# Kernel tuning notes

Measured on AMD Instinct MI355X. Metric: run time of the kernel, lower is better.

The kernel has to match this reference:

```python
import jax, jax.numpy as jnp
import numpy as np
import math

D_MODEL = 1024
D_INNER = 2048
D_HALF = D_INNER // 2
D_STATE = 16
D_CONV = 4
DT_RANK = 64
B_SZ = 4
L = 2048


def _dw_conv(x, w, b):
    # x: (b, l, c), w: (k, 1, c) depthwise, SAME padding
    y = jax.lax.conv_general_dilated(
        x, w, window_strides=(1,), padding='SAME',
        feature_group_count=x.shape[-1],
        dimension_numbers=('NWC', 'WIO', 'NWC'))
    return y + b


def _selective_scan(u, delta, A, Bc, Cc, D):
    # u, delta: (b, l, d); Bc, Cc: (b, l, n); A: (d, n); D: (d,)
    b, l, d = u.shape
    n = A.shape[1]

    def step(h, inp):
        d_t, u_t, B_t, C_t = inp  # (b,d), (b,d), (b,n), (b,n)
        dA = jnp.exp(d_t[..., None] * A)                     # (b,d,n)
        h = dA * h + (d_t * u_t)[..., None] * B_t[:, None, :]
        y = jnp.einsum('bdn,bn->bd', h, C_t)
        return h, y

    h0 = jnp.zeros((b, d, n), u.dtype)
    xs = (jnp.moveaxis(delta, 1, 0), jnp.moveaxis(u, 1, 0),
          jnp.moveaxis(Bc, 1, 0), jnp.moveaxis(Cc, 1, 0))
    _, ys = jax.lax.scan(step, h0, xs)                       # (l,b,d)
    return jnp.moveaxis(ys, 0, 1) + u * D


def setup_inputs() -> dict:
    key = jax.random.key(0)
    ks = jax.random.split(key, 12)
    x = jax.random.normal(ks[0], (B_SZ, L, D_MODEL), jnp.float32)
    W_in = jax.random.normal(ks[1], (D_MODEL, D_INNER), jnp.float32) * (D_MODEL ** -0.5)
    conv_x_w = jax.random.normal(ks[2], (D_CONV, 1, D_HALF), jnp.float32) * (D_CONV ** -0.5)
    conv_x_b = jnp.zeros((D_HALF,), jnp.float32)
    conv_z_w = jax.random.normal(ks[3], (D_CONV, 1, D_HALF), jnp.float32) * (D_CONV ** -0.5)
    conv_z_b = jnp.zeros((D_HALF,), jnp.float32)
    W_xdbl = jax.random.normal(ks[4], (D_HALF, DT_RANK + 2 * D_STATE), jnp.float32) * (D_HALF ** -0.5)
    dt_init_std = DT_RANK ** -0.5  # dt_scale = 1.0
    W_dt = jax.random.uniform(ks[5], (DT_RANK, D_HALF), jnp.float32, -dt_init_std, dt_init_std)
    rand_vals = jax.random.uniform(ks[6], (D_HALF,))
    dt_bias = jnp.exp(rand_vals * (math.log(0.1) - math.log(0.001)) + math.log(0.001))
    dt_bias = jnp.clip(dt_bias, 1e-4)
    inv_dt = dt_bias + jnp.log(-jnp.expm1(-dt_bias))
    D = jnp.ones((D_HALF,), jnp.float32)
    W_out = jax.random.normal(ks[7], (D_INNER, D_MODEL), jnp.float32) * (D_INNER ** -0.5)
    b_out = jnp.zeros((D_MODEL,), jnp.float32)
    return dict(x=x, W_in=W_in, conv_x_w=conv_x_w, conv_x_b=conv_x_b,
                conv_z_w=conv_z_w, conv_z_b=conv_z_b, W_xdbl=W_xdbl,
                W_dt=W_dt, inv_dt=inv_dt, D=D, W_out=W_out, b_out=b_out)


def reference(x, W_in, conv_x_w, conv_x_b, conv_z_w, conv_z_b, W_xdbl,
              W_dt, inv_dt, D, W_out, b_out):
    xz = x @ W_in                                            # (b,l,d_inner), no bias
    xs, z = jnp.split(xz, 2, axis=-1)                        # (b,l,d_half) each
    # A = -exp(log(arange(1..N))) tiled over channels
    A = -jnp.tile(jnp.arange(1, D_STATE + 1, dtype=jnp.float32), (D_HALF, 1))  # (d,n)
    xs = jax.nn.silu(_dw_conv(xs, conv_x_w, conv_x_b))
    z = jax.nn.silu(_dw_conv(z, conv_z_w, conv_z_b))
    x_dbl = xs @ W_xdbl                                      # (b,l,dt_rank+2n)
    dt_low, Bc, Cc = jnp.split(x_dbl, [DT_RANK, DT_RANK + D_STATE], axis=-1)
    dt = dt_low @ W_dt + inv_dt                              # Dense with bias_init=inv_dt
    delta = jax.nn.softplus(dt + inv_dt)                     # scan adds delta_bias=inv_dt again (faithful)
    y = _selective_scan(xs, delta, A, Bc, Cc, D)             # (b,l,d_half)
    y = jnp.concatenate([y, z], axis=-1)                     # (b,l,d_inner)
    return y @ W_out + b_out
```

## Files before the change

### kernel.cpp

```cpp
#include <hip/hip_runtime.h>
#include <hip/hip_bf16.h>
#include <math.h>

#define B_SZ 4
#define LSEQ 2048
#define DM 1024
#define DI 2048
#define DH 1024
#define DS 16
#define DTR 64
#define RTOT 96
#define MROWS (B_SZ * LSEQ)

#define NCH 32
#define CHUNK 64

typedef short bf8_t __attribute__((ext_vector_type(8)));
typedef float f4_t __attribute__((ext_vector_type(4)));

__device__ __forceinline__ unsigned short f2bfbits(float v) {
  __hip_bfloat16 h = __float2bfloat16(v);
  return *(unsigned short*)&h;
}
__device__ __forceinline__ float bfu_lo(unsigned int v) {
  unsigned int x = v << 16;
  return *(float*)&x;
}
__device__ __forceinline__ float bfu_hi(unsigned int v) {
  unsigned int x = v & 0xffff0000u;
  return *(float*)&x;
}

__device__ __forceinline__ void gl_lds16(const void* g, void* l) {
  __builtin_amdgcn_global_load_lds(
      (const __attribute__((address_space(1))) unsigned int*)g,
      (__attribute__((address_space(3))) unsigned int*)l,
      16, 0, 0);
}
__device__ __forceinline__ void gl_lds16_nt(const void* g, void* l) {
  __builtin_amdgcn_global_load_lds(
      (const __attribute__((address_space(1))) unsigned int*)g,
      (__attribute__((address_space(3))) unsigned int*)l,
      16, 0, 2);
}

__device__ __forceinline__ void ld8f(const float* p, unsigned short* d) {
  const float4 a = ((const float4*)p)[0];
  const float4 b = ((const float4*)p)[1];
  d[0] = f2bfbits(a.x); d[1] = f2bfbits(a.y); d[2] = f2bfbits(a.z); d[3] = f2bfbits(a.w);
  d[4] = f2bfbits(b.x); d[5] = f2bfbits(b.y); d[6] = f2bfbits(b.z); d[7] = f2bfbits(b.w);
}

#define VMCNT(n) asm volatile("s_waitcnt vmcnt(" #n ")" ::: "memory")
#define LGKM0 asm volatile("s_waitcnt lgkmcnt(0)" ::: "memory")

__global__ void probe_kernel(const unsigned short* __restrict__ p, int* __restrict__ flag) {
  int lane = threadIdx.x;
  int sane = 0;
#pragma unroll
  for (int j = 0; j < 4; j++) {
    unsigned short lo = p[(lane * 4 + j) * 2];
    int e = (lo >> 7) & 0xFF;
    sane += (e <= 130) ? 1 : 0;
  }
  sane += __shfl_xor(sane, 1, 64);
  sane += __shfl_xor(sane, 2, 64);
  sane += __shfl_xor(sane, 4, 64);
  sane += __shfl_xor(sane, 8, 64);
  sane += __shfl_xor(sane, 16, 64);
  sane += __shfl_xor(sane, 32, 64);
  if (lane == 0) *flag = (sane >= 220) ? 1 : 0;
}

__global__ __launch_bounds__(256) void cast_kernel(
    const int* __restrict__ flag, const float* __restrict__ x,
    unsigned short* __restrict__ xbf) {
  if (*flag == 1) return;
  int i = (blockIdx.x * 256 + threadIdx.x) * 8;
  unsigned short d[8];
  ld8f(x + i, d);
  *(uint4*)&xbf[i] = *(uint4*)d;
}

#define PREP_TOT 78848
__global__ __launch_bounds__(256) void prep_kernel(
    const int* __restrict__ flag,
    const void* s0, const void* s1, const void* s2, const void* s3,
    const void* s4, const void* s5, const void* s6, const void* s7,
    float* __restrict__ out) {
  int i = blockIdx.x * 256 + threadIdx.x;
  if (i >= PREP_TOT) return;
  const void* src; int off;
  if      (i < 4096)   { src = s0; off = i; }
  else if (i < 5120)   { src = s1; off = i - 4096; }
  else if (i < 9216)   { src = s2; off = i - 5120; }
  else if (i < 10240)  { src = s3; off = i - 9216; }
  else if (i < 75776)  { src = s4; off = i - 10240; }
  else if (i < 76800)  { src = s5; off = i - 75776; }
  else if (i < 77824)  { src = s6; off = i - 76800; }
  else                 { src = s7; off = i - 77824; }
  float v = (*flag == 1) ? __bfloat162float(((const __hip_bfloat16*)src)[off])
                         : ((const float*)src)[off];
  out[i] = v;
}

__global__ __launch_bounds__(256) void transpose_kernel(
    const int* __restrict__ flag, const void* __restrict__ W,
    unsigned short* __restrict__ Wt, int K, int N) {
  __shared__ unsigned short tile[32][33];
  int n0 = blockIdx.x * 32, k0 = blockIdx.y * 32;
  int c = threadIdx.x & 31, r8 = threadIdx.x >> 5;
  bool isbf = (*flag == 1);
#pragma unroll
  for (int p = 0; p < 4; p++) {
    int r = r8 + p * 8;
    unsigned short v;
    if (isbf) v = ((const unsigned short*)W)[(size_t)(k0 + r) * N + n0 + c];
    else      v = f2bfbits(((const float*)W)[(size_t)(k0 + r) * N + n0 + c]);
    tile[r][c] = v;
  }
  __syncthreads();
#pragma unroll
  for (int p = 0; p < 4; p++) {
    int r = r8 + p * 8;
    Wt[(size_t)(n0 + r) * K + k0 + c] = tile[c][r];
  }
}

__global__ __launch_bounds__(256) void transpose_pad_kernel(
    const int* __restrict__ flag, const void* __restrict__ W,
    unsigned short* __restrict__ Wt) {
  __shared__ unsigned short tile[32][33];
  int n0 = blockIdx.x * 32, k0 = blockIdx.y * 32;
  int c = threadIdx.x & 31, r8 = threadIdx.x >> 5;
  bool isbf = (*flag == 1);
#pragma unroll
  for (int p = 0; p < 4; p++) {
    int r = r8 + p * 8;
    unsigned short v = 0;
    if (n0 + c < RTOT) {
      if (isbf) v = ((const unsigned short*)W)[(size_t)(k0 + r) * RTOT + n0 + c];
      else      v = f2bfbits(((const float*)W)[(size_t)(k0 + r) * RTOT + n0 + c]);
    }
    tile[r][c] = v;
  }
  __syncthreads();
#pragma unroll
  for (int p = 0; p < 4; p++) {
    int r = r8 + p * 8;
    Wt[(size_t)(n0 + r) * DH + k0 + c] = tile[c][r];
  }
}

template <int BN, bool OUT_BY_FLAG>
__global__ __launch_bounds__(512, 2) void gemm_bk32(
    const int* __restrict__ flag,
    const unsigned short* __restrict__ A1, const unsigned short* __restrict__ A0,
    const unsigned short* __restrict__ Bt,
    const float* __restrict__ bias, void* __restrict__ C,
    int N, int K) {
  extern __shared__ __align__(16) unsigned short lds[];
  constexpr int A_BUF = 256 * 32;
  constexpr int B_BUF = BN * 32;
  constexpr int B_OFF = 4 * A_BUF;
  constexpr int NF = BN / 64;
  constexpr int NB_LD = BN / 128;

  const int flagv = *flag;
  const unsigned short* Ap = (flagv == 1) ? A1 : A0;

  const int tid = threadIdx.x;
  const int lane = tid & 63;
  const int wave = tid >> 6;
  const int quad = lane >> 4;
  const int l16 = lane & 15;
  const int wm = wave >> 2;
  const int wn = wave & 3;

  const int NB = gridDim.x, MB = gridDim.y;
  int L = blockIdx.y * NB + blockIdx.x;
  int xcd = L & 7;
  int w = L >> 3;
  int m_band = xcd * (MB >> 3) + (w / NB);
  int n_blk = w % NB;
  const int m0 = m_band * 256;
  const int n0 = n_blk * BN;

  const int NT = K >> 5;

  f4_t acc[8][NF] = {};

  auto stage = [&](int kt) {
    const int buf = kt & 3;
    const int k0 = kt * 32;
    unsigned short* Ad = lds + buf * A_BUF;
#pragma unroll
    for (int j = 0; j < 2; j++) {
      int ch = tid + j * 512;
      int mi = ch >> 2, s = ch & 3;
      int ki = s ^ ((mi >> 1) & 3);
      gl_lds16_nt(Ap + (size_t)(m0 + mi) * K + k0 + ki * 8,
                  Ad + (j * 512 + wave * 64) * 8);
    }
    unsigned short* Bd = lds + B_OFF + buf * B_BUF;
#pragma unroll
    for (int j = 0; j < NB_LD; j++) {
      int ch = tid + j * 512;
      int ni = ch >> 2, s = ch & 3;
      int ki = s ^ ((ni >> 1) & 3);
      gl_lds16(Bt + (size_t)(n0 + ni) * K + k0 + ki * 8,
               Bd + (j * 512 + wave * 64) * 8);
    }
  };

  stage(0); stage(1); stage(2);

  for (int t = 0; t < NT; t++) {
    if (t + 2 < NT) {
      if constexpr (NF == 4) VMCNT(8); else VMCNT(6);
    } else if (t + 1 < NT) {
      if constexpr (NF == 4) VMCNT(4); else VMCNT(3);
    } else {
      VMCNT(0);
    }
    __builtin_amdgcn_s_barrier();

    const unsigned short* Ac = lds + (t & 3) * A_BUF;
    const unsigned short* Bc = lds + B_OFF + (t & 3) * B_BUF;
    bf8_t af[8], bfr[NF];
#pragma unroll
    for (int ti = 0; ti < 8; ti++) {
      int r = wm * 128 + ti * 16 + l16;
      af[ti] = *(const bf8_t*)&Ac[(r * 4 + (quad ^ ((r >> 1) & 3))) * 8];
    }
#pragma unroll
    for (int tj = 0; tj < NF; tj++) {
      int rn = wn * (BN / 4) + tj * 16 + l16;
      bfr[tj] = *(const bf8_t*)&Bc[(rn * 4 + (quad ^ ((rn >> 1) & 3))) * 8];
    }
    if (t + 3 < NT) stage(t + 3);

    LGKM0;
    __builtin_amdgcn_sched_barrier(0);
    __builtin_amdgcn_s_setprio(1);
#pragma unroll
    for (int ti = 0; ti < 8; ti++)
#pragma unroll
      for (int tj = 0; tj < NF; tj++)
        acc[ti][tj] = __builtin_amdgcn_mfma_f32_16x16x32_bf16(
            af[ti], bfr[tj], acc[ti][tj], 0, 0, 0);
    __builtin_amdgcn_s_setprio(0);
    __builtin_amdgcn_s_barrier();
  }

#pragma unroll
  for (int ti = 0; ti < 8; ti++) {
#pragma unroll
    for (int tj = 0; tj < NF; tj++) {
      int col = n0 + wn * (BN / 4) + tj * 16 + l16;
      float bv = bias ? bias[col] : 0.f;
#pragma unroll
      for (int r = 0; r < 4; r++) {
        int row = m0 + wm * 128 + ti * 16 + quad * 4 + r;
        float v = acc[ti][tj][r] + bv;
        if constexpr (!OUT_BY_FLAG) {
          __builtin_nontemporal_store(f2bfbits(v),
              (unsigned short*)C + (size_t)row * N + col);
        } else {
          if (flagv == 1)
            __builtin_nontemporal_store(f2bfbits(v),
                (unsigned short*)C + (size_t)row * N + col);
          else
            __builtin_nontemporal_store(v, (float*)C + (size_t)row * N + col);
        }
      }
    }
  }
}

__global__ __launch_bounds__(256) void xdbl_kernel(
    const unsigned short* __restrict__ A, const unsigned short* __restrict__ Bt,
    float* __restrict__ xdbl) {
  const int tid = threadIdx.x;
  const int wave = tid >> 6;
  const int lane = tid & 63;
  const int quad = lane >> 4;
  const int l16 = lane & 15;
  const int m0 = blockIdx.x * 32 + (wave & 1) * 16;
  const int c0 = (wave >> 1) * 48;

  f4_t acc[3] = {};
  const unsigned short* Ar = A + (size_t)(m0 + l16) * DH + quad * 8;
  const unsigned short* B0 = Bt + (size_t)(c0 + l16) * DH + quad * 8;
  const unsigned short* B1 = Bt + (size_t)(c0 + 16 + l16) * DH + quad * 8;
  const unsigned short* B2 = Bt + (size_t)(c0 + 32 + l16) * DH + quad * 8;

#pragma unroll 4
  for (int k0 = 0; k0 < DH; k0 += 32) {
    bf8_t af = *(const bf8_t*)(Ar + k0);
    bf8_t b0 = *(const bf8_t*)(B0 + k0);
    bf8_t b1 = *(const bf8_t*)(B1 + k0);
    bf8_t b2 = *(const bf8_t*)(B2 + k0);
    acc[0] = __builtin_amdgcn_mfma_f32_16x16x32_bf16(af, b0, acc[0], 0, 0, 0);
    acc[1] = __builtin_amdgcn_mfma_f32_16x16x32_bf16(af, b1, acc[1], 0, 0, 0);
    acc[2] = __builtin_amdgcn_mfma_f32_16x16x32_bf16(af, b2, acc[2], 0, 0, 0);
  }

#pragma unroll
  for (int tj = 0; tj < 3; tj++) {
    int col = c0 + tj * 16 + l16;
#pragma unroll
    for (int r = 0; r < 4; r++) {
      int row = m0 + quad * 4 + r;
      xdbl[(size_t)row * RTOT + col] = acc[tj][r];
    }
  }
}

__global__ __launch_bounds__(256) void conv_silu_kernel(
    const unsigned short* __restrict__ xz,
    const float* __restrict__ wx, const float* __restrict__ bx,
    const float* __restrict__ wz, const float* __restrict__ bz,
    unsigned short* __restrict__ xs_bf, unsigned short* __restrict__ cat) {
  int gid = blockIdx.x * 256 + threadIdx.x;
  int cg = gid & 127;
  int c0 = cg * 8;
  int m = gid >> 7;
  int t = m & (LSEQ - 1);
  float ax[8], az[8];
#pragma unroll
  for (int i = 0; i < 8; i++) { ax[i] = bx[c0 + i]; az[i] = bz[c0 + i]; }
#pragma unroll
  for (int j = 0; j < 4; j++) {
    int tt = t - 1 + j;
    if (tt < 0 || tt >= LSEQ) continue;
    size_t row = (size_t)(m - t + tt);
    uint4 vx = *(const uint4*)&xz[row * DI + c0];
    uint4 vz = *(const uint4*)&xz[row * DI + DH + c0];
    const unsigned int* px = (const unsigned int*)&vx;
    const unsigned int* pz = (const unsigned int*)&vz;
#pragma unroll
    for (int q = 0; q < 4; q++) {
      float x0 = bfu_lo(px[q]), x1 = bfu_hi(px[q]);
      float z0 = bfu_lo(pz[q]), z1 = bfu_hi(pz[q]);
      ax[q * 2]     = fmaf(wx[j * DH + c0 + q * 2], x0, ax[q * 2]);
      ax[q * 2 + 1] = fmaf(wx[j * DH + c0 + q * 2 + 1], x1, ax[q * 2 + 1]);
      az[q * 2]     = fmaf(wz[j * DH + c0 + q * 2], z0, az[q * 2]);
      az[q * 2 + 1] = fmaf(wz[j * DH + c0 + q * 2 + 1], z1, az[q * 2 + 1]);
    }
  }
  unsigned short sx[8], sz[8];
#pragma unroll
  for (int i = 0; i < 8; i++) {
    float vx = ax[i] / (1.f + __expf(-ax[i]));
    float vz = az[i] / (1.f + __expf(-az[i]));
    sx[i] = f2bfbits(vx);
    sz[i] = f2bfbits(vz);
  }
  *(uint4*)&xs_bf[(size_t)m * DH + c0] = *(uint4*)sx;
  *(uint4*)&cat[(size_t)m * DI + DH + c0] = *(uint4*)sz;
}

__global__ __launch_bounds__(256) void delta_kernel(
    const float* __restrict__ xdbl, const float* __restrict__ Wdt,
    const float* __restrict__ inv_dt, const unsigned short* __restrict__ xs,
    unsigned int* __restrict__ du) {
  const int d = blockIdx.x * 256 + threadIdx.x;
  const int m0 = blockIdx.y * 8;
  __shared__ float xr[8][DTR];
#pragma unroll
  for (int i = 0; i < 2; i++) {
    int e = threadIdx.x + i * 256;
    xr[e >> 6][e & 63] = xdbl[(size_t)(m0 + (e >> 6)) * RTOT + (e & 63)];
  }
  __syncthreads();
  float acc[8];
#pragma unroll
  for (int i = 0; i < 8; i++) acc[i] = 0.f;
  for (int rr = 0; rr < DTR; rr++) {
    float w = Wdt[(size_t)rr * DH + d];
#pragma unroll
    for (int i = 0; i < 8; i++) acc[i] = fmaf(xr[i][rr], w, acc[i]);
  }
  const float bias2 = 2.f * inv_dt[d];
#pragma unroll
  for (int i = 0; i < 8; i++) {
    float v = acc[i] + bias2;
    float sp = (v > 0.f) ? (v + log1pf(__expf(-v))) : log1pf(__expf(v));
    unsigned int lo = f2bfbits(sp);
    unsigned int hi = xs[(size_t)(m0 + i) * DH + d];
    du[(size_t)(m0 + i) * DH + d] = lo | (hi << 16);
  }
}

__global__ __launch_bounds__(256) void scan_pass1(
    const unsigned int* __restrict__ du, const float* __restrict__ xdbl,
    float* __restrict__ Echunks, float* __restrict__ hp) {
  const int tid = threadIdx.x;
  const int d = blockIdx.x * 256 + tid;
  const int c = blockIdx.y, b = blockIdx.z;
  const int row0 = b * LSEQ + c * CHUNK;
  __shared__ float sBC[CHUNK][32];
#pragma unroll
  for (int i = 0; i < 2; i++) {
    int task = tid + i * 256;
    int r = task >> 3, seg = task & 7;
    *(float4*)&sBC[r][seg * 4] =
        *(const float4*)&xdbl[(size_t)(row0 + r) * RTOT + DTR + seg * 4];
  }
  __syncthreads();
  float h[16];
#pragma unroll
  for (int n = 0; n < 16; n++) h[n] = 0.f;
  float E = 1.f;
  for (int t = 0; t < CHUNK; t++) {
    unsigned int v = du[(size_t)(row0 + t) * DH + d];
    float dt = bfu_lo(v), ut = bfu_hi(v);
    float e = __expf(-dt);
    E *= e;
    float dv = dt * ut;
    float p = 1.f;
#pragma unroll
    for (int n = 0; n < 16; n++) {
      p *= e;
      h[n] = fmaf(p, h[n], dv * sBC[t][n]);
    }
  }
  Echunks[((size_t)c * B_SZ + b) * DH + d] = E;
#pragma unroll
  for (int n = 0; n < 16; n++)
    hp[(((size_t)c * B_SZ + b) * 16 + n) * DH + d] = h[n];
}

__global__ __launch_bounds__(256) void scan_pass2(
    const float* __restrict__ Echunks, const float* __restrict__ hp,
    float* __restrict__ hs) {
  int t = blockIdx.x * 256 + threadIdx.x;
  int d = t & 1023;
  int n = (t >> 10) & 15;
  int b = t >> 14;
  float h = 0.f;
  const int k0 = n + 1;
  for (int c = 0; c < NCH; c++) {
    float E = Echunks[((size_t)c * B_SZ + b) * DH + d];
    float a = 1.f, base = E;
    int k = k0;
#pragma unroll
    for (int i = 0; i < 5; i++) {
      if (k & 1) a *= base;
      base *= base;
      k >>= 1;
    }
    size_t idx = (((size_t)c * B_SZ + b) * 16 + n) * DH + d;
    hs[idx] = h;
    h = fmaf(a, h, hp[idx]);
  }
}

__global__ __launch_bounds__(256) void scan_pass3(
    const unsigned int* __restrict__ du, const float* __restrict__ xdbl,
    const float* __restrict__ hs, const float* __restrict__ Dvec,
    __hip_bfloat16* __restrict__ cat) {
  const int tid = threadIdx.x;
  const int d = blockIdx.x * 256 + tid;
  const int c = blockIdx.y, b = blockIdx.z;
  const int row0 = b * LSEQ + c * CHUNK;
  __shared__ float sBC[CHUNK][32];
#pragma unroll
  for (int i = 0; i < 2; i++) {
    int task = tid + i * 256;
    int r = task >> 3, seg = task & 7;
    *(float4*)&sBC[r][seg * 4] =
        *(const float4*)&xdbl[(size_t)(row0 + r) * RTOT + DTR + seg * 4];
  }
  __syncthreads();
  float h[16];
#pragma unroll
  for (int n = 0; n < 16; n++)
    h[n] = hs[(((size_t)c * B_SZ + b) * 16 + n) * DH + d];
  const float Dd = Dvec[d];
  for (int t = 0; t < CHUNK; t++) {
    unsigned int v = du[(size_t)(row0 + t) * DH + d];
    float dt = bfu_lo(v), ut = bfu_hi(v);
    float e = __expf(-dt);
    float dv = dt * ut;
    float p = 1.f, y = 0.f;
#pragma unroll
    for (int n = 0; n < 16; n++) {
      p *= e;
      h[n] = fmaf(p, h[n], dv * sBC[t][n]);
      y = fmaf(h[n], sBC[t][16 + n], y);
    }
    y = fmaf(ut, Dd, y);
    cat[(size_t)(row0 + t) * DI + d] = __float2bfloat16(y);
  }
}

extern "C" void kernel_launch(void* const* d_in, const int* in_sizes, int n_in,
                              void* d_out, int out_size, void* d_ws, size_t ws_size,
                              hipStream_t stream) {
  char* ws = (char*)d_ws;
  __hip_bfloat16* xz  = (__hip_bfloat16*)(ws);
  unsigned int* du    = (unsigned int*)(ws);
  __hip_bfloat16* xs  = (__hip_bfloat16*)(ws + ((size_t)32 << 20));
  unsigned short* xbf = (unsigned short*)(ws + ((size_t)48 << 20));
  __hip_bfloat16* cat = (__hip_bfloat16*)(ws + ((size_t)64 << 20));
  float* xdbl         = (float*)(ws + ((size_t)96 << 20));
  float* Echunks      = (float*)(ws + ((size_t)99 << 20));
  float* hp           = (float*)(ws + ((size_t)100 << 20));
  float* hs           = (float*)(ws + ((size_t)108 << 20));
  unsigned short* Wt_in  = (unsigned short*)(ws + ((size_t)116 << 20));
  unsigned short* Wt_out = (unsigned short*)(ws + ((size_t)120 << 20));
  unsigned short* Wxt    = (unsigned short*)(ws + ((size_t)124 << 20));
  float* cw           = (float*)(ws + ((size_t)125 << 20));
  int* flag           = (int*)(ws + ((size_t)126 << 20));

  const float* conv_xwf = cw + 0;
  const float* conv_xbf = cw + 4096;
  const float* conv_zwf = cw + 5120;
  const float* conv_zbf = cw + 9216;
  const float* Wdtf     = cw + 10240;
  const float* inv_dtf  = cw + 75776;
  const float* Df       = cw + 76800;
  const float* b_outf   = cw + 77824;

  (void)hipFuncSetAttribute(reinterpret_cast<const void*>(&gemm_bk32<256, false>),
                            hipFuncAttributeMaxDynamicSharedMemorySize, 131072);
  (void)hipFuncSetAttribute(reinterpret_cast<const void*>(&gemm_bk32<128, true>),
                            hipFuncAttributeMaxDynamicSharedMemorySize, 98304);

  probe_kernel<<<1, 64, 0, stream>>>((const unsigned short*)d_in[0], flag);
  cast_kernel<<<4096, 256, 0, stream>>>(flag, (const float*)d_in[0], xbf);
  prep_kernel<<<(PREP_TOT + 255) / 256, 256, 0, stream>>>(
      flag, d_in[2], d_in[3], d_in[4], d_in[5], d_in[7], d_in[8], d_in[9],
      d_in[11], cw);
  transpose_kernel<<<dim3(DI / 32, DM / 32), 256, 0, stream>>>(
      flag, d_in[1], Wt_in, DM, DI);
  transpose_kernel<<<dim3(DM / 32, DI / 32), 256, 0, stream>>>(
      flag, d_in[10], Wt_out, DI, DM);
  transpose_pad_kernel<<<dim3(4, DH / 32), 256, 0, stream>>>(flag, d_in[6], Wxt);

  gemm_bk32<256, false><<<dim3(DI / 256, MROWS / 256), 512, 131072, stream>>>(
      flag, (const unsigned short*)d_in[0], xbf, Wt_in,
      (const float*)nullptr, xz, DI, DM);
  conv_silu_kernel<<<(MROWS * 128) / 256, 256, 0, stream>>>(
      (const unsigned short*)xz, conv_xwf, conv_xbf, conv_zwf, conv_zbf,
      (unsigned short*)xs, (unsigned short*)cat);
  xdbl_kernel<<<MROWS / 32, 256, 0, stream>>>(
      (const unsigned short*)xs, Wxt, xdbl);
  delta_kernel<<<dim3(4, MROWS / 8), 256, 0, stream>>>(
      xdbl, Wdtf, inv_dtf, (const unsigned short*)xs, du);
  scan_pass1<<<dim3(4, NCH, B_SZ), 256, 0, stream>>>(du, xdbl, Echunks, hp);
  scan_pass2<<<256, 256, 0, stream>>>(Echunks, hp, hs);
  scan_pass3<<<dim3(4, NCH, B_SZ), 256, 0, stream>>>(du, xdbl, hs, Df, cat);
  gemm_bk32<128, true><<<dim3(DM / 128, MROWS / 256), 512, 98304, stream>>>(
      flag, (const unsigned short*)cat, (const unsigned short*)cat, Wt_out,
      b_outf, d_out, DM, DI);
}
```

Baseline: 375.2 us.

## Compute delta projection with bf16 MFMA using split hi/lo operands

Replaces the scalar FP32 delta projection (dt_low @ W_dt) with an MFMA kernel. The dt_low activations and W_dt weights are each split into bf16 hi and lo parts and laid out along a K=192 axis, so the bf16 products hi*hi + lo*hi + hi*lo come close to FP32 accuracy. The xdbl kernel now writes the split activations directly, and a new kernel builds the transposed split weights. The aim is to move this small-K GEMM onto matrix cores, at the cost of extra workspace traffic, triple the K length, and slight precision loss from dropping the lo*lo term.

```diff
diff --git a/kernel.cpp b/kernel.cpp
--- a/kernel.cpp
+++ b/kernel.cpp
@@ -15,6 +15,8 @@
 #define NCH 32
 #define CHUNK 64
 
+#define KD 192
+
 typedef short bf8_t __attribute__((ext_vector_type(8)));
 typedef float f4_t __attribute__((ext_vector_type(4)));
 
@@ -28,6 +30,10 @@
 }
 __device__ __forceinline__ float bfu_hi(unsigned int v) {
   unsigned int x = v & 0xffff0000u;
+  return *(float*)&x;
+}
+__device__ __forceinline__ float bf16f(unsigned short h) {
+  unsigned int x = ((unsigned int)h) << 16;
   return *(float*)&x;
 }
 
@@ -152,6 +158,31 @@
   }
 }
 
+__global__ __launch_bounds__(256) void wdtt_kernel(
+    const float* __restrict__ Wdt, unsigned short* __restrict__ Wdtt) {
+  __shared__ unsigned short th[32][33], tl[32][33];
+  int n0 = blockIdx.x * 32, k0 = blockIdx.y * 32;
+  int c = threadIdx.x & 31, r8 = threadIdx.x >> 5;
+#pragma unroll
+  for (int p = 0; p < 4; p++) {
+    int r = r8 + p * 8;
+    float w = Wdt[(size_t)(k0 + r) * DH + n0 + c];
+    unsigned short hi = f2bfbits(w);
+    th[r][c] = hi;
+    tl[r][c] = f2bfbits(w - bf16f(hi));
+  }
+  __syncthreads();
+#pragma unroll
+  for (int p = 0; p < 4; p++) {
+    int r = r8 + p * 8;
+    unsigned short hi = th[c][r], lo = tl[c][r];
+    size_t base = (size_t)(n0 + r) * KD + k0 + c;
+    Wdtt[base] = hi;
+    Wdtt[base + 64] = hi;
+    Wdtt[base + 128] = lo;
+  }
+}
+
 template <int BN, bool OUT_BY_FLAG>
 __global__ __launch_bounds__(512, 2) void gemm_bk32(
     const int* __restrict__ flag,
@@ -280,7 +311,7 @@
 
 __global__ __launch_bounds__(256) void xdbl_kernel(
     const unsigned short* __restrict__ A, const unsigned short* __restrict__ Bt,
-    float* __restrict__ xdbl) {
+    float* __restrict__ xdbl, unsigned short* __restrict__ Adelta) {
   const int tid = threadIdx.x;
   const int wave = tid >> 6;
   const int lane = tid & 63;
@@ -312,7 +343,68 @@
 #pragma unroll
     for (int r = 0; r < 4; r++) {
       int row = m0 + quad * 4 + r;
-      xdbl[(size_t)row * RTOT + col] = acc[tj][r];
+      float v = acc[tj][r];
+      if (col < 64) {
+        unsigned short hi = f2bfbits(v);
+        unsigned short lo = f2bfbits(v - bf16f(hi));
+        size_t base = (size_t)row * KD + col;
+        Adelta[base] = hi;
+        Adelta[base + 64] = lo;
+        Adelta[base + 128] = hi;
+      } else {
+        xdbl[(size_t)row * RTOT + col] = v;
+      }
+    }
+  }
+}
+
+__global__ __launch_bounds__(256) void delta_mfma_kernel(
+    const unsigned short* __restrict__ Ad,
+    const unsigned short* __restrict__ Bd,
+    const float* __restrict__ inv_dt,
+    const unsigned short* __restrict__ xs,
+    unsigned int* __restrict__ du) {
+  const int tid = threadIdx.x;
+  const int wave = tid >> 6;
+  const int lane = tid & 63;
+  const int quad = lane >> 4;
+  const int l16 = lane & 15;
+  const int m0 = blockIdx.x * 128 + wave * 32;
+  const int n0 = blockIdx.y * 128;
+
+  f4_t acc[2][8] = {};
+  const unsigned short* Ar0 = Ad + (size_t)(m0 + l16) * KD + quad * 8;
+  const unsigned short* Ar1 = Ad + (size_t)(m0 + 16 + l16) * KD + quad * 8;
+
+#pragma unroll
+  for (int ks = 0; ks < 6; ks++) {
+    const int k0 = ks * 32;
+    bf8_t a0 = *(const bf8_t*)(Ar0 + k0);
+    bf8_t a1 = *(const bf8_t*)(Ar1 + k0);
+#pragma unroll
+    for (int nj = 0; nj < 8; nj++) {
+      bf8_t b = *(const bf8_t*)(Bd + (size_t)(n0 + nj * 16 + l16) * KD + quad * 8 + k0);
+      acc[0][nj] = __builtin_amdgcn_mfma_f32_16x16x32_bf16(a0, b, acc[0][nj], 0, 0, 0);
+      acc[1][nj] = __builtin_amdgcn_mfma_f32_16x16x32_bf16(a1, b, acc[1][nj], 0, 0, 0);
+    }
+  }
+
+#pragma unroll
+  for (int mi = 0; mi < 2; mi++) {
+#pragma unroll
+    for (int nj = 0; nj < 8; nj++) {
+      int col = n0 + nj * 16 + l16;
+      float bias2 = 2.f * inv_dt[col];
+#pragma unroll
+      for (int r = 0; r < 4; r++) {
+        int row = m0 + mi * 16 + quad * 4 + r;
+        float v = acc[mi][nj][r] + bias2;
+        float sp = (v > 0.f) ? (v + __logf(1.f + __expf(-v)))
+                             : __logf(1.f + __expf(v));
+        unsigned int lo = f2bfbits(sp);
+        unsigned int hi = xs[(size_t)row * DH + col];
+        du[(size_t)row * DH + col] = lo | (hi << 16);
+      }
     }
   }
 }
@@ -359,38 +451,6 @@
   }
   *(uint4*)&xs_bf[(size_t)m * DH + c0] = *(uint4*)sx;
   *(uint4*)&cat[(size_t)m * DI + DH + c0] = *(uint4*)sz;
-}
-
-__global__ __launch_bounds__(256) void delta_kernel(
-    const float* __restrict__ xdbl, const float* __restrict__ Wdt,
-    const float* __restrict__ inv_dt, const unsigned short* __restrict__ xs,
-    unsigned int* __restrict__ du) {
-  const int d = blockIdx.x * 256 + threadIdx.x;
-  const int m0 = blockIdx.y * 8;
-  __shared__ float xr[8][DTR];
-#pragma unroll
-  for (int i = 0; i < 2; i++) {
-    int e = threadIdx.x + i * 256;
-    xr[e >> 6][e & 63] = xdbl[(size_t)(m0 + (e >> 6)) * RTOT + (e & 63)];
-  }
-  __syncthreads();
-  float acc[8];
-#pragma unroll
-  for (int i = 0; i < 8; i++) acc[i] = 0.f;
-  for (int rr = 0; rr < DTR; rr++) {
-    float w = Wdt[(size_t)rr * DH + d];
-#pragma unroll
-    for (int i = 0; i < 8; i++) acc[i] = fmaf(xr[i][rr], w, acc[i]);
-  }
-  const float bias2 = 2.f * inv_dt[d];
-#pragma unroll
-  for (int i = 0; i < 8; i++) {
-    float v = acc[i] + bias2;
-    float sp = (v > 0.f) ? (v + log1pf(__expf(-v))) : log1pf(__expf(v));
-    unsigned int lo = f2bfbits(sp);
-    unsigned int hi = xs[(size_t)(m0 + i) * DH + d];
-    du[(size_t)(m0 + i) * DH + d] = lo | (hi << 16);
-  }
 }
 
 __global__ __launch_bounds__(256) void scan_pass1(
@@ -508,7 +568,9 @@
   float* xdbl         = (float*)(ws + ((size_t)96 << 20));
   float* Echunks      = (float*)(ws + ((size_t)99 << 20));
   float* hp           = (float*)(ws + ((size_t)100 << 20));
+  unsigned short* Wdtt = (unsigned short*)(ws + ((size_t)100 << 20));
   float* hs           = (float*)(ws + ((size_t)108 << 20));
+  unsigned short* Adelta = (unsigned short*)(ws + ((size_t)108 << 20));
   unsigned short* Wt_in  = (unsigned short*)(ws + ((size_t)116 << 20));
   unsigned short* Wt_out = (unsigned short*)(ws + ((size_t)120 << 20));
   unsigned short* Wxt    = (unsigned short*)(ws + ((size_t)124 << 20));
@@ -539,6 +601,7 @@
   transpose_kernel<<<dim3(DM / 32, DI / 32), 256, 0, stream>>>(
       flag, d_in[10], Wt_out, DI, DM);
   transpose_pad_kernel<<<dim3(4, DH / 32), 256, 0, stream>>>(flag, d_in[6], Wxt);
+  wdtt_kernel<<<dim3(DH / 32, 2), 256, 0, stream>>>(Wdtf, Wdtt);
 
   gemm_bk32<256, false><<<dim3(DI / 256, MROWS / 256), 512, 131072, stream>>>(
       flag, (const unsigned short*)d_in[0], xbf, Wt_in,
@@ -547,9 +610,9 @@
       (const unsigned short*)xz, conv_xwf, conv_xbf, conv_zwf, conv_zbf,
       (unsigned short*)xs, (unsigned short*)cat);
   xdbl_kernel<<<MROWS / 32, 256, 0, stream>>>(
-      (const unsigned short*)xs, Wxt, xdbl);
-  delta_kernel<<<dim3(4, MROWS / 8), 256, 0, stream>>>(
-      xdbl, Wdtf, inv_dtf, (const unsigned short*)xs, du);
+      (const unsigned short*)xs, Wxt, xdbl, Adelta);
+  delta_mfma_kernel<<<dim3(MROWS / 128, DH / 128), 256, 0, stream>>>(
+      Adelta, Wdtt, inv_dtf, (const unsigned short*)xs, du);
   scan_pass1<<<dim3(4, NCH, B_SZ), 256, 0, stream>>>(du, xdbl, Echunks, hp);
   scan_pass2<<<256, 256, 0, stream>>>(Echunks, hp, hs);
   scan_pass3<<<dim3(4, NCH, B_SZ), 256, 0, stream>>>(du, xdbl, hs, Df, cat);
```

Result: faster. 364.6 us (-2.8%).
